# Performance work log

Measured on AMD Instinct MI355X. Metric: run time of the kernel, lower is better.

The kernel has to match this reference:

```python
import jax, jax.numpy as jnp
import numpy as np

DIM = 64
NUM_NODES = 64
SEQ_LEN = 256
BATCH = 64


def setup_inputs() -> dict:
    key = jax.random.key(0)
    ks = jax.random.split(key, 8)
    D = DIM
    x = jax.random.normal(ks[0], (SEQ_LEN, BATCH, NUM_NODES, D), dtype=jnp.float32)
    mask = jnp.ones((SEQ_LEN,), dtype=jnp.int32)
    # msg MLP: Linear(3D -> D) + GELU
    lim_msg = 1.0 / np.sqrt(3 * D)
    msg_W = jax.random.uniform(ks[1], (D, 3 * D), minval=-lim_msg, maxval=lim_msg, dtype=jnp.float32)
    msg_b = jax.random.uniform(ks[2], (D,), minval=-lim_msg, maxval=lim_msg, dtype=jnp.float32)
    # GRUCell(input=D, hidden=D); torch init U(-1/sqrt(hidden), 1/sqrt(hidden))
    lim_g = 1.0 / np.sqrt(D)
    W_ih = jax.random.uniform(ks[3], (3 * D, D), minval=-lim_g, maxval=lim_g, dtype=jnp.float32)
    W_hh = jax.random.uniform(ks[4], (3 * D, D), minval=-lim_g, maxval=lim_g, dtype=jnp.float32)
    b_ih = jax.random.uniform(ks[5], (3 * D,), minval=-lim_g, maxval=lim_g, dtype=jnp.float32)
    b_hh = jax.random.uniform(ks[6], (3 * D,), minval=-lim_g, maxval=lim_g, dtype=jnp.float32)
    # TimeEncode params
    basis_freq = jnp.asarray(1.0 / 10.0 ** np.linspace(0, 9, D), dtype=jnp.float32)
    phase = jnp.zeros((D,), dtype=jnp.float32)
    return {"x": x, "mask": mask, "msg_W": msg_W, "msg_b": msg_b,
            "W_ih": W_ih, "W_hh": W_hh, "b_ih": b_ih, "b_hh": b_hh,
            "basis_freq": basis_freq, "phase": phase}


def _forward(x, mask, msg_W, msg_b, W_ih, W_hh, b_ih, b_hh, basis_freq, phase):
    T, B, C, D = x.shape
    # TimeEncode: cos(t * freq + phase) -> [T, D]
    ts = jnp.arange(T, dtype=jnp.float32)[:, None]
    t_enc = jnp.cos(ts * basis_freq[None, :] + phase[None, :])
    # init_func == 'mean': mean over time -> [B, C, D] -> [B*C, D]
    s0 = jnp.mean(x, axis=0).reshape(B * C, D)
    # time_range = arange(T) * mask (gather indices)
    tr = jnp.arange(T) * mask.astype(jnp.int32)
    x_seq = x[tr].reshape(T, B * C, D)      # gathered timesteps
    te_seq = t_enc[tr]                       # [T, D]

    def step(s, inp):
        xt, tt = inp                        # xt: [B*C, D], tt: [D]
        tt_b = jnp.broadcast_to(tt[None, :], xt.shape)
        cat = jnp.concatenate([xt, s, tt_b], axis=-1)  # [B*C, 3D]
        msg = jax.nn.gelu(cat @ msg_W.T + msg_b, approximate=False)
        # GRUCell (torch gate order: r, z, n)
        gi = msg @ W_ih.T + b_ih
        gh = s @ W_hh.T + b_hh
        i_r, i_z, i_n = jnp.split(gi, 3, axis=-1)
        h_r, h_z, h_n = jnp.split(gh, 3, axis=-1)
        r = jax.nn.sigmoid(i_r + h_r)
        z = jax.nn.sigmoid(i_z + h_z)
        n = jnp.tanh(i_n + r * h_n)
        s_new = (1.0 - z) * n + z * s
        return s_new, s_new

    _, states = jax.lax.scan(step, s0, (x_seq, te_seq))
    return states.reshape(T, B, C, D)


def reference(x, mask, msg_W, msg_b, W_ih, W_hh, b_ih, b_hh, basis_freq, phase):
    return _forward(x, mask, msg_W, msg_b, W_ih, W_hh, b_ih, b_hh, basis_freq, phase)
```

## Files before the change

### kernel.cpp

```cpp
#include <hip/hip_runtime.h>
#include <math.h>

#define DD    64
#define TT    256
#define NROW  4096
#define BLK   256
#define GRID  256

typedef __attribute__((ext_vector_type(8))) short  short8;
typedef __attribute__((ext_vector_type(4))) float  f32x4;

#define BARRIER() do {                                        \
    asm volatile("s_waitcnt lgkmcnt(0)" ::: "memory");        \
    __builtin_amdgcn_sched_barrier(0);                        \
    __builtin_amdgcn_s_barrier();                             \
    __builtin_amdgcn_sched_barrier(0);                        \
  } while (0)

__device__ __forceinline__ float fexp2(float x) {
  float r;
  asm("v_exp_f32 %0, %1" : "=v"(r) : "v"(x));
  return r;
}

__device__ __forceinline__ unsigned short f2bf(float f) {
  unsigned u = __builtin_bit_cast(unsigned, f);
  u += 0x7fffu + ((u >> 16) & 1u);
  return (unsigned short)(u >> 16);
}

__device__ __forceinline__ unsigned long long pack4(f32x4 v) {
  return (unsigned long long)f2bf(v[0])
       | ((unsigned long long)f2bf(v[1]) << 16)
       | ((unsigned long long)f2bf(v[2]) << 32)
       | ((unsigned long long)f2bf(v[3]) << 48);
}

__device__ __forceinline__ short8 pack_frag(f32x4 a, f32x4 b) {
  short8 r;
  r[0] = (short)f2bf(a[0]); r[1] = (short)f2bf(a[1]);
  r[2] = (short)f2bf(a[2]); r[3] = (short)f2bf(a[3]);
  r[4] = (short)f2bf(b[0]); r[5] = (short)f2bf(b[1]);
  r[6] = (short)f2bf(b[2]); r[7] = (short)f2bf(b[3]);
  return r;
}

__device__ __forceinline__ short8 load_wfrag(const float* p) {
  f32x4 a = *(const f32x4*)p;
  f32x4 b = *(const f32x4*)(p + 4);
  return pack_frag(a, b);
}

__device__ __forceinline__ short8 load_wfrag_s(const float* p, float s) {
  f32x4 a = *(const f32x4*)p * s;
  f32x4 b = *(const f32x4*)(p + 4) * s;
  return pack_frag(a, b);
}

__device__ __forceinline__ float ferf(float x) {
  float ax = fabsf(x);
  float t  = __builtin_amdgcn_rcpf(fmaf(0.3275911f, ax, 1.0f));
  float p  = fmaf(1.061405429f, t, -1.453152027f);
  p = fmaf(p, t, 1.421413741f);
  p = fmaf(p, t, -0.284496736f);
  p = fmaf(p, t, 0.254829592f);
  p = p * t;
  float y = 1.0f - p * fexp2(ax * ax * -1.44269504f);
  return copysignf(y, x);
}

__global__ void bias_kernel(const float* __restrict__ msg_W,
                            const float* __restrict__ msg_b,
                            const float* __restrict__ freq,
                            const float* __restrict__ phase,
                            float* __restrict__ bias_t) {
  __shared__ float teL[DD];
  const int t = blockIdx.x;
  const int j = threadIdx.x;
  teL[j] = cosf(fmaf((float)t, freq[j], phase[j]));
  __syncthreads();
  float acc = msg_b[j];
  const float* wrow = msg_W + j * 192 + 128;
  #pragma unroll 8
  for (int k = 0; k < DD; ++k) acc = fmaf(teL[k], wrow[k], acc);
  bias_t[t * DD + j] = acc;
}

__launch_bounds__(BLK, 1)
__global__ void scan9(const float* __restrict__ x,
                      const int*   __restrict__ mask,
                      const float* __restrict__ msg_W,
                      const float* __restrict__ W_ih,
                      const float* __restrict__ W_hh,
                      const float* __restrict__ b_ih,
                      const float* __restrict__ b_hh,
                      const float* __restrict__ bias_t,
                      float* __restrict__ out) {
  __shared__ alignas(16) unsigned short xs[16 * 72];
  __shared__ alignas(16) unsigned short ss[16 * 72];
  __shared__ alignas(16) unsigned short ms[16 * 72];
  __shared__ alignas(16) float s0t[16 * 68];
  __shared__ int tr_lds[TT];

  const int tid  = threadIdx.x;
  const int lane = tid & 63;
  const int wv   = tid >> 6;
  const int col  = lane & 15;
  const int kh   = lane >> 4;
  const int n    = wv * 16 + col;
  const int row0 = blockIdx.x * 16;

  tr_lds[tid] = tid * mask[tid];

  const float SC_RZ = -1.44269504f, SC_N = 2.88539008f;
  short8 wm[4], wi[3][2], wh[3][2];
  {
    const float* mrow = msg_W + (size_t)n * 192;
    #pragma unroll
    for (int kf = 0; kf < 4; ++kf) wm[kf] = load_wfrag(mrow + kf * 32 + kh * 8);
    const float sc[3] = {SC_RZ, SC_RZ, SC_N};
    #pragma unroll
    for (int p = 0; p < 3; ++p) {
      const float* irow = W_ih + (size_t)(p * 64 + n) * 64;
      const float* hrow = W_hh + (size_t)(p * 64 + n) * 64;
      #pragma unroll
      for (int kf = 0; kf < 2; ++kf) {
        wi[p][kf] = load_wfrag_s(irow + kf * 32 + kh * 8, sc[p]);
        wh[p][kf] = load_wfrag_s(hrow + kf * 32 + kh * 8, sc[p]);
      }
    }
  }
  const float bsum0 = (b_ih[n]       + b_hh[n])       * SC_RZ;
  const float bsum1 = (b_ih[64 + n]  + b_hh[64 + n])  * SC_RZ;
  const float bih2  =  b_ih[128 + n] * SC_N;
  const float bhh2  =  b_hh[128 + n] * SC_N;

  const int fr = tid >> 4;
  const int fd = (tid & 15) * 4;

  {
    const float* px = x + (size_t)(row0 + fr) * DD + fd;
    f32x4 a0 = {0.f,0.f,0.f,0.f}, a1 = {0.f,0.f,0.f,0.f};
    #pragma unroll 4
    for (int t = 0; t < TT; t += 2) {
      a0 += *(const f32x4*)(px + (size_t)t * (NROW * DD));
      a1 += *(const f32x4*)(px + (size_t)(t + 1) * (NROW * DD));
    }
    f32x4 m = (a0 + a1) * (1.0f / 256.0f);
    *(f32x4*)&s0t[fr * 68 + fd] = m;
    *(unsigned long long*)&ss[fr * 72 + fd] = pack4(m);
    f32x4 xv0 = *(const f32x4*)px;
    *(unsigned long long*)&xs[fr * 72 + fd] = pack4(xv0);
  }
  __syncthreads();

  float s_reg[4];
  #pragma unroll
  for (int i = 0; i < 4; ++i) s_reg[i] = s0t[(kh * 4 + i) * 68 + n];
  float btc = bias_t[n];

  f32x4 xvA = {0.f,0.f,0.f,0.f}, xvB = {0.f,0.f,0.f,0.f};
  xvA = *(const f32x4*)(x + ((size_t)tr_lds[1] * NROW + row0 + fr) * DD + fd);

  auto body = [&](int t, f32x4& xv_use, f32x4& xv_load) {
    if (t + 2 < TT)
      xv_load = *(const f32x4*)(x + ((size_t)tr_lds[t + 2] * NROW + row0 + fr) * DD + fd);
    float btn = 0.f;
    if (t + 1 < TT) btn = bias_t[tr_lds[t + 1] * DD + n];

    const unsigned short* ax = &xs[(lane & 15) * 72];
    const unsigned short* as = &ss[(lane & 15) * 72];
    short8 xa0 = *(const short8*)(ax + kh * 8);
    short8 xa1 = *(const short8*)(ax + 32 + kh * 8);
    short8 sa0 = *(const short8*)(as + kh * 8);
    short8 sa1 = *(const short8*)(as + 32 + kh * 8);

    f32x4 amx = {0.f,0.f,0.f,0.f};
    amx = __builtin_amdgcn_mfma_f32_16x16x32_bf16(xa0, wm[0], amx, 0, 0, 0);
    amx = __builtin_amdgcn_mfma_f32_16x16x32_bf16(xa1, wm[1], amx, 0, 0, 0);
    f32x4 ams = {0.f,0.f,0.f,0.f};
    ams = __builtin_amdgcn_mfma_f32_16x16x32_bf16(sa0, wm[2], ams, 0, 0, 0);
    ams = __builtin_amdgcn_mfma_f32_16x16x32_bf16(sa1, wm[3], ams, 0, 0, 0);
    f32x4 agh[3];
    #pragma unroll
    for (int p = 0; p < 3; ++p) {
      f32x4 c = {0.f,0.f,0.f,0.f};
      c = __builtin_amdgcn_mfma_f32_16x16x32_bf16(sa0, wh[p][0], c, 0, 0, 0);
      c = __builtin_amdgcn_mfma_f32_16x16x32_bf16(sa1, wh[p][1], c, 0, 0, 0);
      agh[p] = c;
    }

    #pragma unroll
    for (int i = 0; i < 4; ++i) {
      float a = amx[i] + ams[i] + btc;
      float g = 0.5f * a * (1.0f + ferf(a * 0.70710678118654752f));
      ms[(kh * 4 + i) * 72 + n] = f2bf(g);
    }
    btc = btn;
    BARRIER();

    const unsigned short* am = &ms[(lane & 15) * 72];
    short8 ma0 = *(const short8*)(am + kh * 8);
    short8 ma1 = *(const short8*)(am + 32 + kh * 8);
    f32x4 agi[3];
    #pragma unroll
    for (int p = 0; p < 3; ++p) {
      f32x4 c = {0.f,0.f,0.f,0.f};
      c = __builtin_amdgcn_mfma_f32_16x16x32_bf16(ma0, wi[p][0], c, 0, 0, 0);
      c = __builtin_amdgcn_mfma_f32_16x16x32_bf16(ma1, wi[p][1], c, 0, 0, 0);
      agi[p] = c;
    }

    #pragma unroll
    for (int i = 0; i < 4; ++i) {
      const int rr = kh * 4 + i;
      float er = agi[0][i] + agh[0][i] + bsum0;
      float ez = agi[1][i] + agh[1][i] + bsum1;
      float rg = __builtin_amdgcn_rcpf(1.0f + fexp2(er));
      float zg = __builtin_amdgcn_rcpf(1.0f + fexp2(ez));
      float yn = fmaf(rg, agh[2][i] + bhh2, agi[2][i] + bih2);
      float ng = 1.0f - 2.0f * __builtin_amdgcn_rcpf(1.0f + fexp2(yn));
      float sn = fmaf(zg, s_reg[i] - ng, ng);
      s_reg[i] = sn;
      ss[rr * 72 + n] = f2bf(sn);
      out[((size_t)t * NROW + row0 + rr) * DD + n] = sn;
    }
    if (t + 1 < TT)
      *(unsigned long long*)&xs[fr * 72 + fd] = pack4(xv_use);
    BARRIER();
  };

  for (int tt = 0; tt < TT; tt += 2) {
    body(tt,     xvA, xvB);
    body(tt + 1, xvB, xvA);
  }
}

extern "C" void kernel_launch(void* const* d_in, const int* in_sizes, int n_in,
                              void* d_out, int out_size, void* d_ws, size_t ws_size,
                              hipStream_t stream) {
  const float* x      = (const float*)d_in[0];
  const int*   mask   = (const int*)  d_in[1];
  const float* msg_W  = (const float*)d_in[2];
  const float* msg_b  = (const float*)d_in[3];
  const float* W_ih   = (const float*)d_in[4];
  const float* W_hh   = (const float*)d_in[5];
  const float* b_ih   = (const float*)d_in[6];
  const float* b_hh   = (const float*)d_in[7];
  const float* freq   = (const float*)d_in[8];
  const float* phase  = (const float*)d_in[9];
  float* out    = (float*)d_out;
  float* bias_t = (float*)d_ws;

  (void)in_sizes; (void)n_in; (void)out_size; (void)ws_size;

  bias_kernel<<<TT, DD, 0, stream>>>(msg_W, msg_b, freq, phase, bias_t);
  scan9<<<GRID, BLK, 0, stream>>>(x, mask, msg_W, W_ih, W_hh,
                                  b_ih, b_hh, bias_t, out);
}
```

Baseline: 360.4 us.

## Run each 16-row recurrence in a single wavefront to eliminate block barriers

The scan kernel shrinks from four wavefronts to one wavefront per 16-row tile. Each lane now computes all 64 output columns using transposed MFMAs, so the two s_barrier synchronisations per timestep go away. W_hh moves to LDS as bf16, and the state and message tiles are exchanged through padded packed-bf16 LDS buffers. Output is staged in LDS and written a step later with coalesced vector stores, and bf16 conversion switches to the hardware v_cvt_pk_bf16_f32 instruction. The cost is a 4x serial MFMA and transcendental load per wave, higher register pressure, and only one wave per CU, which reduces latency hiding.

```diff
diff --git a/kernel.cpp b/kernel.cpp
--- a/kernel.cpp
+++ b/kernel.cpp
@@ -4,59 +4,41 @@
 #define DD    64
 #define TT    256
 #define NROW  4096
-#define BLK   256
+#define BLK   64
 #define GRID  256
 
 typedef __attribute__((ext_vector_type(8))) short  short8;
 typedef __attribute__((ext_vector_type(4))) float  f32x4;
-
-#define BARRIER() do {                                        \
-    asm volatile("s_waitcnt lgkmcnt(0)" ::: "memory");        \
-    __builtin_amdgcn_sched_barrier(0);                        \
-    __builtin_amdgcn_s_barrier();                             \
-    __builtin_amdgcn_sched_barrier(0);                        \
-  } while (0)
 
 __device__ __forceinline__ float fexp2(float x) {
   float r;
   asm("v_exp_f32 %0, %1" : "=v"(r) : "v"(x));
   return r;
 }
-
-__device__ __forceinline__ unsigned short f2bf(float f) {
-  unsigned u = __builtin_bit_cast(unsigned, f);
-  u += 0x7fffu + ((u >> 16) & 1u);
-  return (unsigned short)(u >> 16);
-}
-
-__device__ __forceinline__ unsigned long long pack4(f32x4 v) {
-  return (unsigned long long)f2bf(v[0])
-       | ((unsigned long long)f2bf(v[1]) << 16)
-       | ((unsigned long long)f2bf(v[2]) << 32)
-       | ((unsigned long long)f2bf(v[3]) << 48);
-}
-
+__device__ __forceinline__ unsigned cvtpk(float lo, float hi) {
+  unsigned r;
+  asm("v_cvt_pk_bf16_f32 %0, %1, %2" : "=v"(r) : "v"(lo), "v"(hi));
+  return r;
+}
+__device__ __forceinline__ unsigned short f2bf1(float f) {
+  return (unsigned short)cvtpk(f, f);
+}
 __device__ __forceinline__ short8 pack_frag(f32x4 a, f32x4 b) {
-  short8 r;
-  r[0] = (short)f2bf(a[0]); r[1] = (short)f2bf(a[1]);
-  r[2] = (short)f2bf(a[2]); r[3] = (short)f2bf(a[3]);
-  r[4] = (short)f2bf(b[0]); r[5] = (short)f2bf(b[1]);
-  r[6] = (short)f2bf(b[2]); r[7] = (short)f2bf(b[3]);
-  return r;
-}
-
+  union { unsigned u[4]; short8 s; } z;
+  z.u[0] = cvtpk(a[0], a[1]); z.u[1] = cvtpk(a[2], a[3]);
+  z.u[2] = cvtpk(b[0], b[1]); z.u[3] = cvtpk(b[2], b[3]);
+  return z.s;
+}
 __device__ __forceinline__ short8 load_wfrag(const float* p) {
   f32x4 a = *(const f32x4*)p;
   f32x4 b = *(const f32x4*)(p + 4);
   return pack_frag(a, b);
 }
-
 __device__ __forceinline__ short8 load_wfrag_s(const float* p, float s) {
   f32x4 a = *(const f32x4*)p * s;
   f32x4 b = *(const f32x4*)(p + 4) * s;
   return pack_frag(a, b);
 }
-
 __device__ __forceinline__ float ferf(float x) {
   float ax = fabsf(x);
   float t  = __builtin_amdgcn_rcpf(fmaf(0.3275911f, ax, 1.0f));
@@ -69,11 +51,14 @@
   return copysignf(y, x);
 }
 
-__global__ void bias_kernel(const float* __restrict__ msg_W,
-                            const float* __restrict__ msg_b,
-                            const float* __restrict__ freq,
-                            const float* __restrict__ phase,
-                            float* __restrict__ bias_t) {
+#define SC_RZ (-1.44269504f)
+#define SC_N  ( 2.88539008f)
+
+__global__ void bias2_kernel(const float* __restrict__ msg_W,
+                             const float* __restrict__ msg_b,
+                             const float* __restrict__ freq,
+                             const float* __restrict__ phase,
+                             float* __restrict__ bias2) {
   __shared__ float teL[DD];
   const int t = blockIdx.x;
   const int j = threadIdx.x;
@@ -83,156 +68,231 @@
   const float* wrow = msg_W + j * 192 + 128;
   #pragma unroll 8
   for (int k = 0; k < DD; ++k) acc = fmaf(teL[k], wrow[k], acc);
-  bias_t[t * DD + j] = acc;
+  const int jt = j >> 4, jj = j & 15;
+  const int kh = jj >> 2, i = jj & 3;
+  bias2[t * DD + kh * 16 + jt * 4 + i] = acc;
 }
 
 __launch_bounds__(BLK, 1)
-__global__ void scan9(const float* __restrict__ x,
-                      const int*   __restrict__ mask,
-                      const float* __restrict__ msg_W,
-                      const float* __restrict__ W_ih,
-                      const float* __restrict__ W_hh,
-                      const float* __restrict__ b_ih,
-                      const float* __restrict__ b_hh,
-                      const float* __restrict__ bias_t,
-                      float* __restrict__ out) {
-  __shared__ alignas(16) unsigned short xs[16 * 72];
-  __shared__ alignas(16) unsigned short ss[16 * 72];
-  __shared__ alignas(16) unsigned short ms[16 * 72];
-  __shared__ alignas(16) float s0t[16 * 68];
-  __shared__ int tr_lds[TT];
-
-  const int tid  = threadIdx.x;
-  const int lane = tid & 63;
-  const int wv   = tid >> 6;
-  const int col  = lane & 15;
+__global__ void scan12(const float* __restrict__ x,
+                       const int*   __restrict__ mask,
+                       const float* __restrict__ msg_W,
+                       const float* __restrict__ W_ih,
+                       const float* __restrict__ W_hh,
+                       const float* __restrict__ b_ih,
+                       const float* __restrict__ b_hh,
+                       const float* __restrict__ bias2,
+                       float* __restrict__ out) {
+  __shared__ alignas(16) unsigned short whh_l[192 * 72];
+  __shared__ unsigned int SP[544];
+  __shared__ unsigned int MP[544];
+  __shared__ alignas(16) float outT[16 * 68];
+  __shared__ alignas(16) float biasL[4 * 64];
+
+  const int lane = threadIdx.x;
+  const int r16  = lane & 15;
   const int kh   = lane >> 4;
-  const int n    = wv * 16 + col;
   const int row0 = blockIdx.x * 16;
 
-  tr_lds[tid] = tid * mask[tid];
-
-  const float SC_RZ = -1.44269504f, SC_N = 2.88539008f;
-  short8 wm[4], wi[3][2], wh[3][2];
   {
-    const float* mrow = msg_W + (size_t)n * 192;
-    #pragma unroll
-    for (int kf = 0; kf < 4; ++kf) wm[kf] = load_wfrag(mrow + kf * 32 + kh * 8);
+    biasL[lane]       = (b_ih[lane]       + b_hh[lane])       * SC_RZ;
+    biasL[64 + lane]  = (b_ih[64 + lane]  + b_hh[64 + lane])  * SC_RZ;
+    biasL[128 + lane] =  b_ih[128 + lane] * SC_N;
+    biasL[192 + lane] =  b_hh[128 + lane] * SC_N;
+  }
+  for (int q = 0; q < 192; ++q) {
+    float v = W_hh[q * 64 + lane] * ((q < 128) ? SC_RZ : SC_N);
+    whh_l[q * 72 + lane] = f2bf1(v);
+  }
+  short8 wmx[4][2], wms[4][2], wia[3][4][2];
+  #pragma unroll
+  for (int jt = 0; jt < 4; ++jt) {
+    const float* mrow = msg_W + (size_t)(jt * 16 + r16) * 192;
+    #pragma unroll
+    for (int ks = 0; ks < 2; ++ks) {
+      wmx[jt][ks] = load_wfrag(mrow + ks * 32 + kh * 8);
+      wms[jt][ks] = load_wfrag(mrow + 64 + ks * 32 + kh * 8);
+    }
+  }
+  {
     const float sc[3] = {SC_RZ, SC_RZ, SC_N};
     #pragma unroll
-    for (int p = 0; p < 3; ++p) {
-      const float* irow = W_ih + (size_t)(p * 64 + n) * 64;
-      const float* hrow = W_hh + (size_t)(p * 64 + n) * 64;
-      #pragma unroll
-      for (int kf = 0; kf < 2; ++kf) {
-        wi[p][kf] = load_wfrag_s(irow + kf * 32 + kh * 8, sc[p]);
-        wh[p][kf] = load_wfrag_s(hrow + kf * 32 + kh * 8, sc[p]);
-      }
-    }
-  }
-  const float bsum0 = (b_ih[n]       + b_hh[n])       * SC_RZ;
-  const float bsum1 = (b_ih[64 + n]  + b_hh[64 + n])  * SC_RZ;
-  const float bih2  =  b_ih[128 + n] * SC_N;
-  const float bhh2  =  b_hh[128 + n] * SC_N;
-
-  const int fr = tid >> 4;
-  const int fd = (tid & 15) * 4;
+    for (int p = 0; p < 3; ++p)
+      #pragma unroll
+      for (int qt = 0; qt < 4; ++qt) {
+        const float* irow = W_ih + (size_t)(p * 64 + qt * 16 + r16) * 64;
+        #pragma unroll
+        for (int ks = 0; ks < 2; ++ks)
+          wia[p][qt][ks] = load_wfrag_s(irow + ks * 32 + kh * 8, sc[p]);
+      }
+  }
 
   {
-    const float* px = x + (size_t)(row0 + fr) * DD + fd;
-    f32x4 a0 = {0.f,0.f,0.f,0.f}, a1 = {0.f,0.f,0.f,0.f};
+    f32x4 ac[4][2] = {{{0,0,0,0},{0,0,0,0}},{{0,0,0,0},{0,0,0,0}},
+                      {{0,0,0,0},{0,0,0,0}},{{0,0,0,0},{0,0,0,0}}};
+    const float* px = x + (size_t)(row0 + r16) * DD + kh * 16;
+    const size_t tstep = (size_t)NROW * DD;
     #pragma unroll 4
     for (int t = 0; t < TT; t += 2) {
-      a0 += *(const f32x4*)(px + (size_t)t * (NROW * DD));
-      a1 += *(const f32x4*)(px + (size_t)(t + 1) * (NROW * DD));
-    }
-    f32x4 m = (a0 + a1) * (1.0f / 256.0f);
-    *(f32x4*)&s0t[fr * 68 + fd] = m;
-    *(unsigned long long*)&ss[fr * 72 + fd] = pack4(m);
-    f32x4 xv0 = *(const f32x4*)px;
-    *(unsigned long long*)&xs[fr * 72 + fd] = pack4(xv0);
-  }
-  __syncthreads();
-
-  float s_reg[4];
+      const float* p0 = px + (size_t)t * tstep;
+      const float* p1 = p0 + tstep;
+      #pragma unroll
+      for (int c = 0; c < 4; ++c) {
+        ac[c][0] += *(const f32x4*)(p0 + c * 4);
+        ac[c][1] += *(const f32x4*)(p1 + c * 4);
+      }
+    }
+    #pragma unroll
+    for (int c = 0; c < 4; ++c) {
+      f32x4 m = (ac[c][0] + ac[c][1]) * (1.0f / 256.0f);
+      *(f32x4*)&outT[r16 * 68 + kh * 16 + c * 4] = m;
+      SP[(kh * 8 + c * 2 + 0) * 17 + r16] = cvtpk(m[0], m[1]);
+      SP[(kh * 8 + c * 2 + 1) * 17 + r16] = cvtpk(m[2], m[3]);
+    }
+  }
+  f32x4 s_f[4];
   #pragma unroll
-  for (int i = 0; i < 4; ++i) s_reg[i] = s0t[(kh * 4 + i) * 68 + n];
-  float btc = bias_t[n];
-
-  f32x4 xvA = {0.f,0.f,0.f,0.f}, xvB = {0.f,0.f,0.f,0.f};
-  xvA = *(const f32x4*)(x + ((size_t)tr_lds[1] * NROW + row0 + fr) * DD + fd);
-
-  auto body = [&](int t, f32x4& xv_use, f32x4& xv_load) {
-    if (t + 2 < TT)
-      xv_load = *(const f32x4*)(x + ((size_t)tr_lds[t + 2] * NROW + row0 + fr) * DD + fd);
-    float btn = 0.f;
-    if (t + 1 < TT) btn = bias_t[tr_lds[t + 1] * DD + n];
-
-    const unsigned short* ax = &xs[(lane & 15) * 72];
-    const unsigned short* as = &ss[(lane & 15) * 72];
-    short8 xa0 = *(const short8*)(ax + kh * 8);
-    short8 xa1 = *(const short8*)(ax + 32 + kh * 8);
-    short8 sa0 = *(const short8*)(as + kh * 8);
-    short8 sa1 = *(const short8*)(as + 32 + kh * 8);
-
-    f32x4 amx = {0.f,0.f,0.f,0.f};
-    amx = __builtin_amdgcn_mfma_f32_16x16x32_bf16(xa0, wm[0], amx, 0, 0, 0);
-    amx = __builtin_amdgcn_mfma_f32_16x16x32_bf16(xa1, wm[1], amx, 0, 0, 0);
-    f32x4 ams = {0.f,0.f,0.f,0.f};
-    ams = __builtin_amdgcn_mfma_f32_16x16x32_bf16(sa0, wm[2], ams, 0, 0, 0);
-    ams = __builtin_amdgcn_mfma_f32_16x16x32_bf16(sa1, wm[3], ams, 0, 0, 0);
-    f32x4 agh[3];
-    #pragma unroll
-    for (int p = 0; p < 3; ++p) {
-      f32x4 c = {0.f,0.f,0.f,0.f};
-      c = __builtin_amdgcn_mfma_f32_16x16x32_bf16(sa0, wh[p][0], c, 0, 0, 0);
-      c = __builtin_amdgcn_mfma_f32_16x16x32_bf16(sa1, wh[p][1], c, 0, 0, 0);
-      agh[p] = c;
-    }
-
-    #pragma unroll
-    for (int i = 0; i < 4; ++i) {
-      float a = amx[i] + ams[i] + btc;
-      float g = 0.5f * a * (1.0f + ferf(a * 0.70710678118654752f));
-      ms[(kh * 4 + i) * 72 + n] = f2bf(g);
-    }
-    btc = btn;
-    BARRIER();
-
-    const unsigned short* am = &ms[(lane & 15) * 72];
-    short8 ma0 = *(const short8*)(am + kh * 8);
-    short8 ma1 = *(const short8*)(am + 32 + kh * 8);
-    f32x4 agi[3];
-    #pragma unroll
-    for (int p = 0; p < 3; ++p) {
-      f32x4 c = {0.f,0.f,0.f,0.f};
-      c = __builtin_amdgcn_mfma_f32_16x16x32_bf16(ma0, wi[p][0], c, 0, 0, 0);
-      c = __builtin_amdgcn_mfma_f32_16x16x32_bf16(ma1, wi[p][1], c, 0, 0, 0);
-      agi[p] = c;
-    }
-
-    #pragma unroll
-    for (int i = 0; i < 4; ++i) {
-      const int rr = kh * 4 + i;
-      float er = agi[0][i] + agh[0][i] + bsum0;
-      float ez = agi[1][i] + agh[1][i] + bsum1;
-      float rg = __builtin_amdgcn_rcpf(1.0f + fexp2(er));
-      float zg = __builtin_amdgcn_rcpf(1.0f + fexp2(ez));
-      float yn = fmaf(rg, agh[2][i] + bhh2, agi[2][i] + bih2);
-      float ng = 1.0f - 2.0f * __builtin_amdgcn_rcpf(1.0f + fexp2(yn));
-      float sn = fmaf(zg, s_reg[i] - ng, ng);
-      s_reg[i] = sn;
-      ss[rr * 72 + n] = f2bf(sn);
-      out[((size_t)t * NROW + row0 + rr) * DD + n] = sn;
-    }
-    if (t + 1 < TT)
-      *(unsigned long long*)&xs[fr * 72 + fd] = pack4(xv_use);
-    BARRIER();
+  for (int qt = 0; qt < 4; ++qt)
+    s_f[qt] = *(const f32x4*)&outT[r16 * 68 + qt * 16 + 4 * kh];
+
+  int tr1 = 1 * mask[1];
+  int tr2 = 2 * mask[2];
+  f32x4 XA[4], XB[4], BA[4], BB[4];
+  {
+    const float* p0 = x + (size_t)(row0 + r16) * DD + kh * 8;
+    XA[0] = *(const f32x4*)p0;        XA[1] = *(const f32x4*)(p0 + 4);
+    XA[2] = *(const f32x4*)(p0 + 32); XA[3] = *(const f32x4*)(p0 + 36);
+    const float* p1 = x + ((size_t)tr1 * NROW + row0 + r16) * DD + kh * 8;
+    XB[0] = *(const f32x4*)p1;        XB[1] = *(const f32x4*)(p1 + 4);
+    XB[2] = *(const f32x4*)(p1 + 32); XB[3] = *(const f32x4*)(p1 + 36);
+    const float* pb = bias2 + kh * 16;
+    #pragma unroll
+    for (int jt = 0; jt < 4; ++jt) BA[jt] = *(const f32x4*)(pb + jt * 4);
+  }
+
+  auto body = [&](int t, f32x4 (&xu)[4], f32x4 (&bu)[4], f32x4 (&bl)[4]) {
+    if (t > 0) {
+      #pragma unroll
+      for (int q = 0; q < 4; ++q) {
+        f32x4 ov = *(const f32x4*)&outT[(q * 4 + kh) * 68 + r16 * 4];
+        *(f32x4*)(out + ((size_t)(t - 1) * NROW + row0 + q * 4 + kh) * DD + r16 * 4) = ov;
+      }
+    }
+    short8 xB0 = pack_frag(xu[0], xu[1]);
+    short8 xB1 = pack_frag(xu[2], xu[3]);
+    {
+      const float* pn = x + ((size_t)tr2 * NROW + row0 + r16) * DD + kh * 8;
+      xu[0] = *(const f32x4*)pn;        xu[1] = *(const f32x4*)(pn + 4);
+      xu[2] = *(const f32x4*)(pn + 32); xu[3] = *(const f32x4*)(pn + 36);
+    }
+    {
+      const float* pb = bias2 + (size_t)tr1 * DD + kh * 16;
+      #pragma unroll
+      for (int jt = 0; jt < 4; ++jt) bl[jt] = *(const f32x4*)(pb + jt * 4);
+    }
+    tr1 = tr2;
+    {
+      int t3 = t + 3;
+      tr2 = (t3 < TT) ? t3 * mask[t3] : 0;
+    }
+
+    short8 sB0, sB1;
+    {
+      union { unsigned u[4]; short8 s; } z0, z1;
+      const int base = 4 * kh * 17 + r16;
+      #pragma unroll
+      for (int w = 0; w < 4; ++w) {
+        z0.u[w] = SP[base + w * 17];
+        z1.u[w] = SP[base + (16 + w) * 17];
+      }
+      sB0 = z0.s; sB1 = z1.s;
+    }
+
+    f32x4 ghC[4][3];
+    #pragma unroll
+    for (int qt = 0; qt < 4; ++qt) {
+      f32x4 bnh = *(const f32x4*)&biasL[192 + qt * 16 + 4 * kh];
+      #pragma unroll
+      for (int p = 0; p < 3; ++p) {
+        const unsigned short* wrow = &whh_l[(p * 64 + qt * 16 + r16) * 72];
+        short8 a0 = *(const short8*)(wrow + kh * 8);
+        short8 a1 = *(const short8*)(wrow + 32 + kh * 8);
+        f32x4 c = (p == 2) ? bnh : f32x4{0.f, 0.f, 0.f, 0.f};
+        c = __builtin_amdgcn_mfma_f32_16x16x32_bf16(a0, sB0, c, 0, 0, 0);
+        c = __builtin_amdgcn_mfma_f32_16x16x32_bf16(a1, sB1, c, 0, 0, 0);
+        ghC[qt][p] = c;
+      }
+    }
+
+    #pragma unroll
+    for (int jt = 0; jt < 4; ++jt) {
+      f32x4 c = {0.f, 0.f, 0.f, 0.f};
+      c = __builtin_amdgcn_mfma_f32_16x16x32_bf16(wmx[jt][0], xB0, c, 0, 0, 0);
+      c = __builtin_amdgcn_mfma_f32_16x16x32_bf16(wmx[jt][1], xB1, c, 0, 0, 0);
+      c = __builtin_amdgcn_mfma_f32_16x16x32_bf16(wms[jt][0], sB0, c, 0, 0, 0);
+      c = __builtin_amdgcn_mfma_f32_16x16x32_bf16(wms[jt][1], sB1, c, 0, 0, 0);
+      float g0, g1, g2, g3;
+      {
+        float a0 = c[0] + bu[jt][0], a1 = c[1] + bu[jt][1];
+        float a2 = c[2] + bu[jt][2], a3 = c[3] + bu[jt][3];
+        g0 = 0.5f * a0 * (1.0f + ferf(a0 * 0.70710678118654752f));
+        g1 = 0.5f * a1 * (1.0f + ferf(a1 * 0.70710678118654752f));
+        g2 = 0.5f * a2 * (1.0f + ferf(a2 * 0.70710678118654752f));
+        g3 = 0.5f * a3 * (1.0f + ferf(a3 * 0.70710678118654752f));
+      }
+      MP[(jt * 8 + 2 * kh + 0) * 17 + r16] = cvtpk(g0, g1);
+      MP[(jt * 8 + 2 * kh + 1) * 17 + r16] = cvtpk(g2, g3);
+    }
+
+    short8 mB0, mB1;
+    {
+      union { unsigned u[4]; short8 s; } z0, z1;
+      const int base = 4 * kh * 17 + r16;
+      #pragma unroll
+      for (int w = 0; w < 4; ++w) {
+        z0.u[w] = MP[base + w * 17];
+        z1.u[w] = MP[base + (16 + w) * 17];
+      }
+      mB0 = z0.s; mB1 = z1.s;
+    }
+
+    #pragma unroll
+    for (int qt = 0; qt < 4; ++qt) {
+      f32x4 gR = *(const f32x4*)&biasL[qt * 16 + 4 * kh];
+      f32x4 gZ = *(const f32x4*)&biasL[64 + qt * 16 + 4 * kh];
+      f32x4 gN = *(const f32x4*)&biasL[128 + qt * 16 + 4 * kh];
+      gR = __builtin_amdgcn_mfma_f32_16x16x32_bf16(wia[0][qt][0], mB0, gR, 0, 0, 0);
+      gR = __builtin_amdgcn_mfma_f32_16x16x32_bf16(wia[0][qt][1], mB1, gR, 0, 0, 0);
+      gZ = __builtin_amdgcn_mfma_f32_16x16x32_bf16(wia[1][qt][0], mB0, gZ, 0, 0, 0);
+      gZ = __builtin_amdgcn_mfma_f32_16x16x32_bf16(wia[1][qt][1], mB1, gZ, 0, 0, 0);
+      gN = __builtin_amdgcn_mfma_f32_16x16x32_bf16(wia[2][qt][0], mB0, gN, 0, 0, 0);
+      gN = __builtin_amdgcn_mfma_f32_16x16x32_bf16(wia[2][qt][1], mB1, gN, 0, 0, 0);
+      f32x4 sn;
+      #pragma unroll
+      for (int i = 0; i < 4; ++i) {
+        float er = gR[i] + ghC[qt][0][i];
+        float ez = gZ[i] + ghC[qt][1][i];
+        float rg = __builtin_amdgcn_rcpf(1.0f + fexp2(er));
+        float zg = __builtin_amdgcn_rcpf(1.0f + fexp2(ez));
+        float yn = fmaf(rg, ghC[qt][2][i], gN[i]);
+        float ng = 1.0f - 2.0f * __builtin_amdgcn_rcpf(1.0f + fexp2(yn));
+        sn[i] = fmaf(zg, s_f[qt][i] - ng, ng);
+      }
+      s_f[qt] = sn;
+      SP[(qt * 8 + 2 * kh + 0) * 17 + r16] = cvtpk(sn[0], sn[1]);
+      SP[(qt * 8 + 2 * kh + 1) * 17 + r16] = cvtpk(sn[2], sn[3]);
+      *(f32x4*)&outT[r16 * 68 + qt * 16 + 4 * kh] = sn;
+    }
   };
 
   for (int tt = 0; tt < TT; tt += 2) {
-    body(tt,     xvA, xvB);
-    body(tt + 1, xvB, xvA);
+    body(tt,     XA, BA, BB);
+    body(tt + 1, XB, BB, BA);
+  }
+  #pragma unroll
+  for (int q = 0; q < 4; ++q) {
+    f32x4 ov = *(const f32x4*)&outT[(q * 4 + kh) * 68 + r16 * 4];
+    *(f32x4*)(out + ((size_t)(TT - 1) * NROW + row0 + q * 4 + kh) * DD + r16 * 4) = ov;
   }
 }
 
@@ -249,12 +309,12 @@
   const float* b_hh   = (const float*)d_in[7];
   const float* freq   = (const float*)d_in[8];
   const float* phase  = (const float*)d_in[9];
-  float* out    = (float*)d_out;
-  float* bias_t = (float*)d_ws;
+  float* out   = (float*)d_out;
+  float* bias2 = (float*)d_ws;
 
   (void)in_sizes; (void)n_in; (void)out_size; (void)ws_size;
 
-  bias_kernel<<<TT, DD, 0, stream>>>(msg_W, msg_b, freq, phase, bias_t);
-  scan9<<<GRID, BLK, 0, stream>>>(x, mask, msg_W, W_ih, W_hh,
-                                  b_ih, b_hh, bias_t, out);
-}
+  bias2_kernel<<<TT, DD, 0, stream>>>(msg_W, msg_b, freq, phase, bias2);
+  scan12<<<GRID, BLK, 0, stream>>>(x, mask, msg_W, W_ih, W_hh,
+                                   b_ih, b_hh, bias2, out);
+}
```

After: 701.5 us. 94.6% more time.
